# Performance work log

Hardware: AMD Instinct MI355X
Metric: run time of the kernel (lower is better)

The kernel has to match this reference:

```python
import jax, jax.numpy as jnp
import numpy as np

B, N, D = 2, 256, 256  # module only type-checks when n_tokens == dim
EPS = 1e-5


def _ln(x, gamma, beta):
    m = jnp.mean(x, axis=-1, keepdims=True)
    v = jnp.var(x, axis=-1, keepdims=True)
    return (x - m) * jax.lax.rsqrt(v + EPS) * gamma + beta


def setup_inputs() -> dict:
    key = jax.random.key(0)
    k0, k1, k2, k3 = jax.random.split(key, 4)
    s = 1.0 / np.sqrt(D).astype(np.float32)
    return {
        "pair_repr": jax.random.normal(k0, (B, N, N, D), jnp.float32),
        "w_in": jax.random.normal(k1, (2 * D, D), jnp.float32) * s,
        "w_gate": jax.random.normal(k2, (D, D), jnp.float32) * s,
        "w_out": jax.random.normal(k3, (D, D), jnp.float32) * s,
        "ln_gamma": jnp.ones((D,), jnp.float32),
        "ln_beta": jnp.zeros((D,), jnp.float32),
    }


def reference(pair_repr, w_in, w_gate, w_out, ln_gamma, ln_beta):
    # shared LayerNorm applied to input
    x = _ln(pair_repr, ln_gamma, ln_beta)                      # [B,N,N,D]
    ab = jnp.einsum('bnid,ed->bnie', x, w_in)                  # [B,N,N,2D]
    a, b = jnp.split(ab, 2, axis=-1)
    a = jax.nn.sigmoid(a) * a                                  # SiLU
    b = jax.nn.sigmoid(b) * b
    g = jax.nn.sigmoid(jnp.einsum('bnid,ed->bnie', x, w_gate))  # [B,N,N,D]
    # 'incoming' pattern: torch.einsum('...ki,...kj->...ij') with ellipsis = (B, N);
    # contracts over the second token axis k, i/j index the channel axis (needs N == D).
    tri = jnp.einsum('bnki,bnkj->bnij', a, b)                  # [B,N,D,D]
    out = jnp.einsum('bnij,ej->bnie', _ln(tri, ln_gamma, ln_beta), w_out)
    return out * g
```

## Files before the change

### kernel.cpp

```cpp
#include <hip/hip_runtime.h>
#include <hip/hip_bf16.h>

typedef __attribute__((ext_vector_type(4))) float  f32x4;
typedef __attribute__((ext_vector_type(8))) short  s16x8;
typedef __attribute__((ext_vector_type(4))) short  s16x4;

union BH4 { s16x4 v; __hip_bfloat16 h[4]; };
union BH8 { s16x8 v; __hip_bfloat16 h[8]; };

#define MFMA16(A,B,C) __builtin_amdgcn_mfma_f32_16x16x32_bf16((A),(B),(C),0,0,0)

__device__ __forceinline__ float sigm(float x) { return 1.0f / (1.0f + __expf(-x)); }

__device__ __forceinline__ int xad(int r, int byteInRow) {
  return ((r << 9) + byteInRow) ^ ((r & 7) << 4);
}
__device__ __forceinline__ int cad64(int i, int k) {
  return (i << 7) + ((((k >> 3) ^ (i & 7)) << 4) | ((k & 7) << 1));
}

__global__ void wfrag_kernel(const float* __restrict__ w_in,
                             const float* __restrict__ w_gate,
                             const float* __restrict__ w_out,
                             __hip_bfloat16* __restrict__ dst) {
  const int lane = threadIdx.x;
  const int fid  = blockIdx.x;
  const int m    = blockIdx.y;
  const float* src = (m == 0) ? w_in : (m == 1) ? (w_in + 65536)
                    : (m == 2) ? w_gate : w_out;
  const int e  = (fid >> 3) * 16 + (lane & 15);
  const int d0 = (fid & 7) * 32 + (lane >> 4) * 8;
  BH8 u;
  #pragma unroll
  for (int j = 0; j < 8; ++j) u.h[j] = __float2bfloat16(src[e * 256 + d0 + j]);
  *reinterpret_cast<s16x8*>(dst + (size_t)m * 65536 + ((size_t)fid * 64 + lane) * 8) = u.v;
}

__global__ __launch_bounds__(256) void ln_kernel(
    const float* __restrict__ pair, const float* __restrict__ gamma,
    const float* __restrict__ beta, __hip_bfloat16* __restrict__ xws)
{
  __shared__ char Xl[8192];
  const int t  = threadIdx.x;
  const int s  = blockIdx.x >> 4;
  const int rt = blockIdx.x & 15;
  const int r  = t >> 4;
  const int c0 = (t & 15) * 16;
  const float* src = pair + (((size_t)s * 256 + rt * 16 + r) * 256 + c0);
  float v[16];
  #pragma unroll
  for (int i = 0; i < 4; ++i) {
    const float4 f = *reinterpret_cast<const float4*>(src + i * 4);
    v[i*4+0]=f.x; v[i*4+1]=f.y; v[i*4+2]=f.z; v[i*4+3]=f.w;
  }
  float sm = 0.f, ss = 0.f;
  #pragma unroll
  for (int i = 0; i < 16; ++i) { sm += v[i]; ss += v[i]*v[i]; }
  #pragma unroll
  for (int m = 1; m < 16; m <<= 1) { sm += __shfl_xor(sm, m); ss += __shfl_xor(ss, m); }
  const float mean = sm * (1.f/256.f);
  const float rstd = rsqrtf(ss * (1.f/256.f) - mean*mean + 1e-5f);
  #pragma unroll
  for (int i = 0; i < 4; ++i) {
    const float4 gm = *reinterpret_cast<const float4*>(gamma + c0 + i*4);
    const float4 bt = *reinterpret_cast<const float4*>(beta  + c0 + i*4);
    BH4 o;
    o.h[0] = __float2bfloat16((v[i*4+0]-mean)*rstd*gm.x + bt.x);
    o.h[1] = __float2bfloat16((v[i*4+1]-mean)*rstd*gm.y + bt.y);
    o.h[2] = __float2bfloat16((v[i*4+2]-mean)*rstd*gm.z + bt.z);
    o.h[3] = __float2bfloat16((v[i*4+3]-mean)*rstd*gm.w + bt.w);
    *reinterpret_cast<s16x4*>(Xl + xad(r, (c0 + i*4)*2)) = o.v;
  }
  __syncthreads();
  #pragma unroll
  for (int p = 0; p < 2; ++p) {
    const int u  = t + p * 256;
    const int ks = u >> 6;
    const int lp = u & 63;
    const s16x8 f = *reinterpret_cast<const s16x8*>(
        Xl + xad(lp & 15, ks*64 + ((lp>>4)&3)*16));
    *reinterpret_cast<s16x8*>(xws + ((((size_t)s*16 + rt)*8 + ks)*64 + lp)*8) = f;
  }
}

__global__ __launch_bounds__(512, 2) void tri_fused(
    const __hip_bfloat16* __restrict__ xws,
    const __hip_bfloat16* __restrict__ wfrag,
    const float* __restrict__ gamma, const float* __restrict__ beta,
    float* __restrict__ out)
{
  extern __shared__ __align__(16) char lds[];
  char* const XS = lds;
  char* const AC = lds + 32768;
  char* const BC = lds + 49152;
  char* const SW = lds;

  const int raw = blockIdx.x;
  const int xcd = raw & 7, o = raw >> 3;
  const int s   = xcd * 64 + (o >> 1);
  const int h   = o & 1;

  const int tid = threadIdx.x, lane = tid & 63, w = tid >> 6;
  const int l15 = lane & 15, lh = lane >> 4;

  const __hip_bfloat16* const wa = wfrag;
  const __hip_bfloat16* const wb = wfrag + 65536;
  const __hip_bfloat16* const wg = wfrag + 131072;
  const __hip_bfloat16* const wo = wfrag + 196608;
  const __hip_bfloat16* const xs = xws + (size_t)s * 65536;

  f32x4 tri[16];
  #pragma unroll
  for (int jt = 0; jt < 16; ++jt) tri[jt] = (f32x4){0.f,0.f,0.f,0.f};

  {
    s16x8 st[4];
    #pragma unroll
    for (int p = 0; p < 4; ++p)
      st[p] = *reinterpret_cast<const s16x8*>(xs + p*4096 + tid*8);
    #pragma unroll
    for (int p = 0; p < 4; ++p)
      *reinterpret_cast<s16x8*>(XS + p*8192 + tid*16) = st[p];
  }
  __syncthreads();

  for (int c = 0; c < 4; ++c) {
    {
      const int ct = h*8 + w;
      f32x4 acc[4];
      #pragma unroll
      for (int rt = 0; rt < 4; ++rt) acc[rt] = (f32x4){0.f,0.f,0.f,0.f};
      #pragma unroll
      for (int ks = 0; ks < 8; ++ks) {
        const s16x8 Bf = *reinterpret_cast<const s16x8*>(wa + (((size_t)ct*8 + ks)*64 + lane)*8);
        #pragma unroll
        for (int rt = 0; rt < 4; ++rt) {
          const s16x8 Af = *reinterpret_cast<const s16x8*>(XS + ((rt*8 + ks)*64 + lane)*16);
          acc[rt] = MFMA16(Af, Bf, acc[rt]);
        }
      }
      #pragma unroll
      for (int rt = 0; rt < 4; ++rt) {
        const f32x4 vv = acc[rt];
        BH4 ov;
        #pragma unroll
        for (int q = 0; q < 4; ++q) ov.h[q] = __float2bfloat16(vv[q] * sigm(vv[q]));
        *reinterpret_cast<s16x4*>(AC + cad64(w*16 + l15, rt*16 + lh*4)) = ov.v;
      }
    }
    #pragma unroll
    for (int t = 0; t < 2; ++t) {
      const int ct = 2*w + t;
      f32x4 acc[4];
      #pragma unroll
      for (int rt = 0; rt < 4; ++rt) acc[rt] = (f32x4){0.f,0.f,0.f,0.f};
      #pragma unroll
      for (int ks = 0; ks < 8; ++ks) {
        const s16x8 Bf = *reinterpret_cast<const s16x8*>(wb + (((size_t)ct*8 + ks)*64 + lane)*8);
        #pragma unroll
        for (int rt = 0; rt < 4; ++rt) {
          const s16x8 Af = *reinterpret_cast<const s16x8*>(XS + ((rt*8 + ks)*64 + lane)*16);
          acc[rt] = MFMA16(Af, Bf, acc[rt]);
        }
      }
      #pragma unroll
      for (int rt = 0; rt < 4; ++rt) {
        const f32x4 vv = acc[rt];
        BH4 ov;
        #pragma unroll
        for (int q = 0; q < 4; ++q) ov.h[q] = __float2bfloat16(vv[q] * sigm(vv[q]));
        *reinterpret_cast<s16x4*>(BC + cad64(ct*16 + l15, rt*16 + lh*4)) = ov.v;
      }
    }
    __syncthreads();

    s16x8 st[4];
    if (c < 3) {
      #pragma unroll
      for (int p = 0; p < 4; ++p)
        st[p] = *reinterpret_cast<const s16x8*>(xs + (c+1)*16384 + p*4096 + tid*8);
    }
    #pragma unroll
    for (int kss = 0; kss < 2; ++kss) {
      const s16x8 ta = *reinterpret_cast<const s16x8*>(AC + cad64(w*16 + l15, kss*32 + lh*8));
      #pragma unroll
      for (int jt = 0; jt < 16; ++jt) {
        const s16x8 tb = *reinterpret_cast<const s16x8*>(BC + cad64(jt*16 + l15, kss*32 + lh*8));
        tri[jt] = MFMA16(ta, tb, tri[jt]);
      }
    }
    if (c < 3) {
      #pragma unroll
      for (int p = 0; p < 4; ++p)
        *reinterpret_cast<s16x8*>(XS + p*8192 + tid*16) = st[p];
    }
    __syncthreads();
  }

  {
    float mean[4], rstd[4];
    #pragma unroll
    for (int q = 0; q < 4; ++q) {
      float sm = 0.f, ss = 0.f;
      #pragma unroll
      for (int jt = 0; jt < 16; ++jt) { const float x = tri[jt][q]; sm += x; ss += x*x; }
      #pragma unroll
      for (int m = 1; m < 16; m <<= 1) { sm += __shfl_xor(sm, m); ss += __shfl_xor(ss, m); }
      mean[q] = sm * (1.f/256.f);
      rstd[q] = rsqrtf(ss * (1.f/256.f) - mean[q]*mean[q] + 1e-5f);
    }
    #pragma unroll
    for (int jt = 0; jt < 16; ++jt) {
      const float gm = gamma[jt*16 + l15];
      const float bt = beta [jt*16 + l15];
      #pragma unroll
      for (int q = 0; q < 4; ++q) {
        const float vv = (tri[jt][q] - mean[q]) * rstd[q] * gm + bt;
        *reinterpret_cast<__hip_bfloat16*>(
            SW + xad(w*16 + lh*4 + q, (jt*16 + l15)*2)) = __float2bfloat16(vv);
      }
    }
  }
  __syncthreads();

  #pragma unroll
  for (int half = 0; half < 2; ++half) {
    #pragma unroll
    for (int t = 0; t < 2; ++t) {
      const int ct = 2*w + t;
      f32x4 og[4], oo[4];
      #pragma unroll
      for (int rt = 0; rt < 4; ++rt) { og[rt] = (f32x4){0.f,0.f,0.f,0.f}; oo[rt] = (f32x4){0.f,0.f,0.f,0.f}; }
      #pragma unroll
      for (int ks = 0; ks < 8; ++ks) {
        const s16x8 Bg = *reinterpret_cast<const s16x8*>(wg + (((size_t)ct*8 + ks)*64 + lane)*8);
        const s16x8 Bo = *reinterpret_cast<const s16x8*>(wo + (((size_t)ct*8 + ks)*64 + lane)*8);
        #pragma unroll
        for (int rt = 0; rt < 4; ++rt) {
          const int rtg = h*8 + half*4 + rt;
          const s16x8 Ax  = *reinterpret_cast<const s16x8*>(xs + (((size_t)rtg*8 + ks)*64 + lane)*8);
          const s16x8 Aln = *reinterpret_cast<const s16x8*>(
              SW + xad(half*64 + rt*16 + l15, ks*64 + lh*16));
          og[rt] = MFMA16(Ax,  Bg, og[rt]);
          oo[rt] = MFMA16(Aln, Bo, oo[rt]);
        }
      }
      #pragma unroll
      for (int rt = 0; rt < 4; ++rt) {
        #pragma unroll
        for (int q = 0; q < 4; ++q) {
          const int row = h*128 + half*64 + rt*16 + lh*4 + q;
          out[(size_t)s*65536 + (size_t)row*256 + ct*16 + l15] =
              oo[rt][q] * sigm(og[rt][q]);
        }
      }
    }
  }
}

extern "C" void kernel_launch(void* const* d_in, const int* in_sizes, int n_in,
                              void* d_out, int out_size, void* d_ws, size_t ws_size,
                              hipStream_t stream) {
  const float* pair   = (const float*)d_in[0];
  const float* w_in   = (const float*)d_in[1];
  const float* w_gate = (const float*)d_in[2];
  const float* w_out  = (const float*)d_in[3];
  const float* gamma  = (const float*)d_in[4];
  const float* beta   = (const float*)d_in[5];
  float* out = (float*)d_out;

  __hip_bfloat16* wfrag = (__hip_bfloat16*)d_ws;
  __hip_bfloat16* xws   = (__hip_bfloat16*)((char*)d_ws + 524288);

  (void)in_sizes; (void)n_in; (void)out_size; (void)ws_size;

  hipFuncSetAttribute(reinterpret_cast<const void*>(tri_fused),
                      hipFuncAttributeMaxDynamicSharedMemorySize, 81920);

  wfrag_kernel<<<dim3(128, 4), 64, 0, stream>>>(w_in, w_gate, w_out, wfrag);
  ln_kernel<<<8192, 256, 0, stream>>>(pair, gamma, beta, xws);
  tri_fused<<<1024, 512, 81920, stream>>>(xws, wfrag, gamma, beta, out);
}
```

Before: 228.7 us.

## Load X fragments directly from global instead of staging through LDS

Removes the LDS staging buffer for the layer-normed X tile and has each wave read its A fragments straight from global memory (pre-fragmented layout), dropping the prefetch registers and copy. LDS use falls from 80KB to 64KB static, which can allow higher occupancy. In exchange every wave re-reads the same X fragments from global/L2, so bandwidth and latency on those loads grow.

New measurement: 354.2 us. +54.9%, slower.

```diff
diff --git a/kernel.cpp b/kernel.cpp
--- a/kernel.cpp
+++ b/kernel.cpp
@@ -89,10 +89,9 @@
     const float* __restrict__ gamma, const float* __restrict__ beta,
     float* __restrict__ out)
 {
-  extern __shared__ __align__(16) char lds[];
-  char* const XS = lds;
-  char* const AC = lds + 32768;
-  char* const BC = lds + 49152;
+  __shared__ __align__(16) char lds[65536];
+  char* const AC = lds;
+  char* const BC = lds + 16384;
   char* const SW = lds;
 
   const int raw = blockIdx.x;
@@ -113,17 +112,6 @@
   #pragma unroll
   for (int jt = 0; jt < 16; ++jt) tri[jt] = (f32x4){0.f,0.f,0.f,0.f};
 
-  {
-    s16x8 st[4];
-    #pragma unroll
-    for (int p = 0; p < 4; ++p)
-      st[p] = *reinterpret_cast<const s16x8*>(xs + p*4096 + tid*8);
-    #pragma unroll
-    for (int p = 0; p < 4; ++p)
-      *reinterpret_cast<s16x8*>(XS + p*8192 + tid*16) = st[p];
-  }
-  __syncthreads();
-
   for (int c = 0; c < 4; ++c) {
     {
       const int ct = h*8 + w;
@@ -135,7 +123,8 @@
         const s16x8 Bf = *reinterpret_cast<const s16x8*>(wa + (((size_t)ct*8 + ks)*64 + lane)*8);
         #pragma unroll
         for (int rt = 0; rt < 4; ++rt) {
-          const s16x8 Af = *reinterpret_cast<const s16x8*>(XS + ((rt*8 + ks)*64 + lane)*16);
+          const s16x8 Af = *reinterpret_cast<const s16x8*>(
+              xs + (((size_t)(c*4 + rt)*8 + ks)*64 + lane)*8);
           acc[rt] = MFMA16(Af, Bf, acc[rt]);
         }
       }
@@ -159,7 +148,8 @@
         const s16x8 Bf = *reinterpret_cast<const s16x8*>(wb + (((size_t)ct*8 + ks)*64 + lane)*8);
         #pragma unroll
         for (int rt = 0; rt < 4; ++rt) {
-          const s16x8 Af = *reinterpret_cast<const s16x8*>(XS + ((rt*8 + ks)*64 + lane)*16);
+          const s16x8 Af = *reinterpret_cast<const s16x8*>(
+              xs + (((size_t)(c*4 + rt)*8 + ks)*64 + lane)*8);
           acc[rt] = MFMA16(Af, Bf, acc[rt]);
         }
       }
@@ -174,12 +164,6 @@
     }
     __syncthreads();
 
-    s16x8 st[4];
-    if (c < 3) {
-      #pragma unroll
-      for (int p = 0; p < 4; ++p)
-        st[p] = *reinterpret_cast<const s16x8*>(xs + (c+1)*16384 + p*4096 + tid*8);
-    }
     #pragma unroll
     for (int kss = 0; kss < 2; ++kss) {
       const s16x8 ta = *reinterpret_cast<const s16x8*>(AC + cad64(w*16 + l15, kss*32 + lh*8));
@@ -188,11 +172,6 @@
         const s16x8 tb = *reinterpret_cast<const s16x8*>(BC + cad64(jt*16 + l15, kss*32 + lh*8));
         tri[jt] = MFMA16(ta, tb, tri[jt]);
       }
-    }
-    if (c < 3) {
-      #pragma unroll
-      for (int p = 0; p < 4; ++p)
-        *reinterpret_cast<s16x8*>(XS + p*8192 + tid*16) = st[p];
     }
     __syncthreads();
   }
@@ -274,10 +253,7 @@
 
   (void)in_sizes; (void)n_in; (void)out_size; (void)ws_size;
 
-  hipFuncSetAttribute(reinterpret_cast<const void*>(tri_fused),
-                      hipFuncAttributeMaxDynamicSharedMemorySize, 81920);
-
   wfrag_kernel<<<dim3(128, 4), 64, 0, stream>>>(w_in, w_gate, w_out, wfrag);
   ln_kernel<<<8192, 256, 0, stream>>>(pair, gamma, beta, xws);
-  tri_fused<<<1024, 512, 81920, stream>>>(xws, wfrag, gamma, beta, out);
-}
+  tri_fused<<<1024, 512, 0, stream>>>(xws, wfrag, gamma, beta, out);
+}
```

## Split pipeline into LN+projection kernel and triangle kernel via workspace

Applied to the files above, without the earlier changes.

Adds a new path that fuses LayerNorm with the a/b/gate projections and SiLU/sigmoid in one kernel, writing bf16 a, b and gate tensors to a large workspace. A second kernel then runs the triangular contraction, the second LayerNorm, the output projection and the gating. This stops the old fused kernel from recomputing the projections once per half-block and lets each kernel run with higher occupancy. The cost is roughly 200MB of extra global traffic for the intermediates, and the new path is only taken when the workspace is large enough; otherwise the old kernels run.

New measurement: 239.6 us. 1.05x slower.

```diff
diff --git a/kernel.cpp b/kernel.cpp
--- a/kernel.cpp
+++ b/kernel.cpp
@@ -36,6 +36,240 @@
   *reinterpret_cast<s16x8*>(dst + (size_t)m * 65536 + ((size_t)fid * 64 + lane) * 8) = u.v;
 }
 
+__global__ __launch_bounds__(512, 4) void k2_lnabg(
+    const float* __restrict__ pair,
+    const __hip_bfloat16* __restrict__ wfrag,
+    const float* __restrict__ gamma, const float* __restrict__ beta,
+    __hip_bfloat16* __restrict__ aT, __hip_bfloat16* __restrict__ bT,
+    __hip_bfloat16* __restrict__ gws)
+{
+  __shared__ __align__(16) char lds[65536];
+  const int raw = blockIdx.x;
+  const int s   = (raw & 7) * 64 + (raw >> 3);
+  const int tid = threadIdx.x, lane = tid & 63, w = tid >> 6;
+  const int l15 = lane & 15, lh = lane >> 4;
+  char* const XW = lds + w * 8192;
+
+  const float4 gm = *reinterpret_cast<const float4*>(gamma + lane * 4);
+  const float4 bt = *reinterpret_cast<const float4*>(beta  + lane * 4);
+
+  s16x8 xr[2][8];
+  #pragma unroll
+  for (int rt = 0; rt < 2; ++rt) {
+    #pragma unroll 1
+    for (int rr = 0; rr < 16; ++rr) {
+      const int r = w * 32 + rt * 16 + rr;
+      const float4 v = *reinterpret_cast<const float4*>(
+          pair + ((size_t)s * 256 + r) * 256 + lane * 4);
+      float sm = v.x + v.y + v.z + v.w;
+      float ss = v.x*v.x + v.y*v.y + v.z*v.z + v.w*v.w;
+      #pragma unroll
+      for (int m = 1; m < 64; m <<= 1) { sm += __shfl_xor(sm, m); ss += __shfl_xor(ss, m); }
+      const float mean = sm * (1.f/256.f);
+      const float rstd = rsqrtf(ss * (1.f/256.f) - mean*mean + 1e-5f);
+      BH4 o;
+      o.h[0] = __float2bfloat16((v.x - mean) * rstd * gm.x + bt.x);
+      o.h[1] = __float2bfloat16((v.y - mean) * rstd * gm.y + bt.y);
+      o.h[2] = __float2bfloat16((v.z - mean) * rstd * gm.z + bt.z);
+      o.h[3] = __float2bfloat16((v.w - mean) * rstd * gm.w + bt.w);
+      *reinterpret_cast<s16x4*>(XW + xad(rr, lane * 8)) = o.v;
+    }
+    #pragma unroll
+    for (int ks = 0; ks < 8; ++ks)
+      xr[rt][ks] = *reinterpret_cast<const s16x8*>(XW + xad(l15, ks*64 + lh*16));
+  }
+
+  #pragma unroll 1
+  for (int cg = 0; cg < 48; ++cg) {
+    const int m  = cg >> 4;
+    const int ct = cg & 15;
+    f32x4 acc0 = (f32x4){0.f,0.f,0.f,0.f};
+    f32x4 acc1 = (f32x4){0.f,0.f,0.f,0.f};
+    #pragma unroll
+    for (int ks = 0; ks < 8; ++ks) {
+      const s16x8 Bf = *reinterpret_cast<const s16x8*>(
+          wfrag + ((size_t)cg * 8 + ks) * 512 + lane * 8);
+      acc0 = MFMA16(xr[0][ks], Bf, acc0);
+      acc1 = MFMA16(xr[1][ks], Bf, acc1);
+    }
+    if (m < 2) {
+      __hip_bfloat16* const dst = (m == 0) ? aT : bT;
+      #pragma unroll
+      for (int rt = 0; rt < 2; ++rt) {
+        const f32x4 a = rt ? acc1 : acc0;
+        BH4 o;
+        #pragma unroll
+        for (int q = 0; q < 4; ++q) o.h[q] = __float2bfloat16(a[q] * sigm(a[q]));
+        const int lane2 = l15 + 16 * ((rt*2 + (lh >> 1)) & 3);
+        *reinterpret_cast<s16x4*>(
+            dst + (((size_t)s*16 + ct)*8 + w)*512 + lane2*8 + (lh & 1)*4) = o.v;
+      }
+    } else {
+      #pragma unroll
+      for (int rt = 0; rt < 2; ++rt) {
+        const f32x4 a = rt ? acc1 : acc0;
+        BH4 o;
+        #pragma unroll
+        for (int q = 0; q < 4; ++q) o.h[q] = __float2bfloat16(sigm(a[q]));
+        const int rtg = w * 2 + rt;
+        *reinterpret_cast<s16x4*>(
+            gws + (((size_t)s*16 + rtg)*16 + ct)*256 + lane*4) = o.v;
+      }
+    }
+  }
+}
+
+__global__ __launch_bounds__(512, 4) void k3_tri(
+    const __hip_bfloat16* __restrict__ aT, const __hip_bfloat16* __restrict__ bT,
+    const __hip_bfloat16* __restrict__ gws, const __hip_bfloat16* __restrict__ wfrag,
+    const float* __restrict__ gamma, const float* __restrict__ beta,
+    float* __restrict__ out)
+{
+  extern __shared__ __align__(16) char lds[];
+  char*  const STG = lds;
+  char*  const SW  = lds;
+  float* const ST  = (float*)(lds + 65536);
+
+  const int raw = blockIdx.x;
+  const int s   = (raw & 7) * 64 + ((raw >> 3) >> 1);
+  const int h   = (raw >> 3) & 1;
+  const int tid = threadIdx.x, lane = tid & 63, w = tid >> 6;
+  const int l15 = lane & 15, lh = lane >> 4;
+  const int r2 = w >> 1, ch = w & 1;
+
+  f32x4 tri[2][8];
+  #pragma unroll
+  for (int rt = 0; rt < 2; ++rt)
+    #pragma unroll
+    for (int t = 0; t < 8; ++t) tri[rt][t] = (f32x4){0.f,0.f,0.f,0.f};
+
+  const int f0 = w * 3;
+  s16x8 stg[3];
+  #pragma unroll
+  for (int p = 0; p < 3; ++p) {
+    const int f = f0 + p;
+    const __hip_bfloat16* src = (f < 8)
+        ? aT + (((size_t)s*16 + h*8 + f)*8 + 0)*512
+        : bT + (((size_t)s*16 + (f-8))*8 + 0)*512;
+    stg[p] = *reinterpret_cast<const s16x8*>(src + lane*8);
+  }
+
+  for (int c = 0; c < 8; ++c) {
+    #pragma unroll
+    for (int p = 0; p < 3; ++p)
+      *reinterpret_cast<s16x8*>(STG + (f0 + p)*1024 + lane*16) = stg[p];
+    __syncthreads();
+    if (c < 7) {
+      #pragma unroll
+      for (int p = 0; p < 3; ++p) {
+        const int f = f0 + p;
+        const __hip_bfloat16* src = (f < 8)
+            ? aT + (((size_t)s*16 + h*8 + f)*8 + (c+1))*512
+            : bT + (((size_t)s*16 + (f-8))*8 + (c+1))*512;
+        stg[p] = *reinterpret_cast<const s16x8*>(src + lane*8);
+      }
+    }
+    const s16x8 ta0 = *reinterpret_cast<const s16x8*>(STG + (r2*2+0)*1024 + lane*16);
+    const s16x8 ta1 = *reinterpret_cast<const s16x8*>(STG + (r2*2+1)*1024 + lane*16);
+    #pragma unroll
+    for (int t = 0; t < 8; ++t) {
+      const s16x8 tb = *reinterpret_cast<const s16x8*>(
+          STG + (8 + ch*8 + t)*1024 + lane*16);
+      tri[0][t] = MFMA16(ta0, tb, tri[0][t]);
+      tri[1][t] = MFMA16(ta1, tb, tri[1][t]);
+    }
+    __syncthreads();
+  }
+
+  float psm[2][4], pss[2][4];
+  #pragma unroll
+  for (int rt = 0; rt < 2; ++rt)
+    #pragma unroll
+    for (int q = 0; q < 4; ++q) {
+      float sm = 0.f, ss = 0.f;
+      #pragma unroll
+      for (int t = 0; t < 8; ++t) { const float v = tri[rt][t][q]; sm += v; ss += v*v; }
+      #pragma unroll
+      for (int m = 1; m < 16; m <<= 1) { sm += __shfl_xor(sm, m); ss += __shfl_xor(ss, m); }
+      psm[rt][q] = sm; pss[rt][q] = ss;
+    }
+  if (l15 == 0) {
+    #pragma unroll
+    for (int rt = 0; rt < 2; ++rt)
+      #pragma unroll
+      for (int q = 0; q < 4; ++q) {
+        const int idx = ((w*2 + rt)*4 + lh)*4 + q;
+        ST[idx*2 + 0] = psm[rt][q];
+        ST[idx*2 + 1] = pss[rt][q];
+      }
+  }
+  __syncthreads();
+  float mean[2][4], rstd[2][4];
+  #pragma unroll
+  for (int rt = 0; rt < 2; ++rt)
+    #pragma unroll
+    for (int q = 0; q < 4; ++q) {
+      const int idx = (((w ^ 1)*2 + rt)*4 + lh)*4 + q;
+      const float sm = psm[rt][q] + ST[idx*2 + 0];
+      const float ss = pss[rt][q] + ST[idx*2 + 1];
+      mean[rt][q] = sm * (1.f/256.f);
+      rstd[rt][q] = rsqrtf(ss * (1.f/256.f) - mean[rt][q]*mean[rt][q] + 1e-5f);
+    }
+  __syncthreads();
+  #pragma unroll
+  for (int t = 0; t < 8; ++t) {
+    const int j = (ch*8 + t)*16 + l15;
+    const float gmv = gamma[j], btv = beta[j];
+    #pragma unroll
+    for (int rt = 0; rt < 2; ++rt)
+      #pragma unroll
+      for (int q = 0; q < 4; ++q) {
+        const int iloc = r2*32 + rt*16 + lh*4 + q;
+        const float v = (tri[rt][t][q] - mean[rt][q]) * rstd[rt][q] * gmv + btv;
+        *reinterpret_cast<__hip_bfloat16*>(SW + xad(iloc, j*2)) = __float2bfloat16(v);
+      }
+  }
+  __syncthreads();
+
+  const __hip_bfloat16* const wo = wfrag + 196608;
+  f32x4 oo[2][8];
+  #pragma unroll
+  for (int rt = 0; rt < 2; ++rt)
+    #pragma unroll
+    for (int t = 0; t < 8; ++t) oo[rt][t] = (f32x4){0.f,0.f,0.f,0.f};
+  #pragma unroll
+  for (int ks = 0; ks < 8; ++ks) {
+    const s16x8 A0 = *reinterpret_cast<const s16x8*>(
+        SW + xad(r2*32 +  0 + l15, ks*64 + lh*16));
+    const s16x8 A1 = *reinterpret_cast<const s16x8*>(
+        SW + xad(r2*32 + 16 + l15, ks*64 + lh*16));
+    #pragma unroll
+    for (int t = 0; t < 8; ++t) {
+      const int cte = ch*8 + t;
+      const s16x8 Bo = *reinterpret_cast<const s16x8*>(
+          wo + ((size_t)(cte*8 + ks))*512 + lane*8);
+      oo[0][t] = MFMA16(A0, Bo, oo[0][t]);
+      oo[1][t] = MFMA16(A1, Bo, oo[1][t]);
+    }
+  }
+  #pragma unroll
+  for (int rt = 0; rt < 2; ++rt) {
+    const int rtg = h*8 + r2*2 + rt;
+    #pragma unroll
+    for (int t = 0; t < 8; ++t) {
+      BH4 gv;
+      gv.v = *reinterpret_cast<const s16x4*>(
+          gws + (((size_t)s*16 + rtg)*16 + (ch*8 + t))*256 + lane*4);
+      #pragma unroll
+      for (int q = 0; q < 4; ++q) {
+        const int row = h*128 + r2*32 + rt*16 + lh*4 + q;
+        out[((size_t)s*256 + row)*256 + (ch*8 + t)*16 + l15] =
+            oo[rt][t][q] * __bfloat162float(gv.h[q]);
+      }
+    }
+  }
+}
+
 __global__ __launch_bounds__(256) void ln_kernel(
     const float* __restrict__ pair, const float* __restrict__ gamma,
     const float* __restrict__ beta, __hip_bfloat16* __restrict__ xws)
@@ -83,7 +317,7 @@
   }
 }
 
-__global__ __launch_bounds__(512, 2) void tri_fused(
+__global__ __launch_bounds__(512, 2) void tri_fused_fb(
     const __hip_bfloat16* __restrict__ xws,
     const __hip_bfloat16* __restrict__ wfrag,
     const float* __restrict__ gamma, const float* __restrict__ beta,
@@ -108,6 +342,7 @@
   const __hip_bfloat16* const wg = wfrag + 131072;
   const __hip_bfloat16* const wo = wfrag + 196608;
   const __hip_bfloat16* const xs = xws + (size_t)s * 65536;
+  const char* const xsb = (const char*)xs;
 
   f32x4 tri[16];
   #pragma unroll
@@ -117,7 +352,7 @@
     s16x8 st[4];
     #pragma unroll
     for (int p = 0; p < 4; ++p)
-      st[p] = *reinterpret_cast<const s16x8*>(xs + p*4096 + tid*8);
+      st[p] = *reinterpret_cast<const s16x8*>(xsb + p*8192 + tid*16);
     #pragma unroll
     for (int p = 0; p < 4; ++p)
       *reinterpret_cast<s16x8*>(XS + p*8192 + tid*16) = st[p];
@@ -178,7 +413,7 @@
     if (c < 3) {
       #pragma unroll
       for (int p = 0; p < 4; ++p)
-        st[p] = *reinterpret_cast<const s16x8*>(xs + (c+1)*16384 + p*4096 + tid*8);
+        st[p] = *reinterpret_cast<const s16x8*>(xsb + (c+1)*32768 + p*8192 + tid*16);
     }
     #pragma unroll
     for (int kss = 0; kss < 2; ++kss) {
@@ -269,15 +504,25 @@
   const float* beta   = (const float*)d_in[5];
   float* out = (float*)d_out;
 
+  (void)in_sizes; (void)n_in; (void)out_size;
+
   __hip_bfloat16* wfrag = (__hip_bfloat16*)d_ws;
-  __hip_bfloat16* xws   = (__hip_bfloat16*)((char*)d_ws + 524288);
-
-  (void)in_sizes; (void)n_in; (void)out_size; (void)ws_size;
-
-  hipFuncSetAttribute(reinterpret_cast<const void*>(tri_fused),
-                      hipFuncAttributeMaxDynamicSharedMemorySize, 81920);
 
   wfrag_kernel<<<dim3(128, 4), 64, 0, stream>>>(w_in, w_gate, w_out, wfrag);
-  ln_kernel<<<8192, 256, 0, stream>>>(pair, gamma, beta, xws);
-  tri_fused<<<1024, 512, 81920, stream>>>(xws, wfrag, gamma, beta, out);
-}
+
+  if (ws_size >= 201850880ULL) {
+    __hip_bfloat16* aT  = (__hip_bfloat16*)((char*)d_ws + 524288);
+    __hip_bfloat16* bT  = (__hip_bfloat16*)((char*)d_ws + 524288 + 67108864);
+    __hip_bfloat16* gws = (__hip_bfloat16*)((char*)d_ws + 524288 + 2*67108864);
+    hipFuncSetAttribute(reinterpret_cast<const void*>(k3_tri),
+                        hipFuncAttributeMaxDynamicSharedMemorySize, 67584);
+    k2_lnabg<<<512, 512, 0, stream>>>(pair, wfrag, gamma, beta, aT, bT, gws);
+    k3_tri<<<1024, 512, 67584, stream>>>(aT, bT, gws, wfrag, gamma, beta, out);
+  } else {
+    __hip_bfloat16* xws = (__hip_bfloat16*)((char*)d_ws + 524288);
+    hipFuncSetAttribute(reinterpret_cast<const void*>(tri_fused_fb),
+                        hipFuncAttributeMaxDynamicSharedMemorySize, 81920);
+    ln_kernel<<<8192, 256, 0, stream>>>(pair, gamma, beta, xws);
+    tri_fused_fb<<<1024, 512, 81920, stream>>>(xws, wfrag, gamma, beta, out);
+  }
+}
```
